# Kernel tuning notes

Measured on AMD Instinct MI355X. Metric: run time of the kernel, lower is better.

## Reference

```python
import jax, jax.numpy as jnp
import numpy as np

B, C, H, W = 4, 256, 48, 48
NUM_HEADS = 8
HEAD_DIM = C // NUM_HEADS
LN_EPS = 1e-5


def setup_inputs() -> dict:
    key = jax.random.key(0)
    ks = jax.random.split(key, 12)
    s = 1.0 / np.sqrt(C)
    return {
        "x": jax.random.normal(ks[0], (B, C, H, W), dtype=jnp.float32),
        "context": jax.random.normal(ks[1], (B, C, H, W), dtype=jnp.float32),
        "Wq": jax.random.uniform(ks[2], (C, C), jnp.float32, -s, s),
        "bq": jax.random.uniform(ks[3], (C,), jnp.float32, -s, s),
        "Wk": jax.random.uniform(ks[4], (C, C), jnp.float32, -s, s),
        "bk": jax.random.uniform(ks[5], (C,), jnp.float32, -s, s),
        "Wv": jax.random.uniform(ks[6], (C, C), jnp.float32, -s, s),
        "bv": jax.random.uniform(ks[7], (C,), jnp.float32, -s, s),
        "Wo": jax.random.uniform(ks[8], (C, C), jnp.float32, -s, s),
        "bo": jax.random.uniform(ks[9], (C,), jnp.float32, -s, s),
        "ln_w": jnp.ones((C,), jnp.float32),
        "ln_b": jnp.zeros((C,), jnp.float32),
    }


def reference(x, context, Wq, bq, Wk, bk, Wv, bv, Wo, bo, ln_w, ln_b):
    b, c, h, w = x.shape
    S = h * w
    # [B, S, C] token layout (x.view(B,C,-1).permute(0,2,1))
    x_flat = x.reshape(b, c, S).transpose(0, 2, 1)
    ctx_flat = context.reshape(b, c, S).transpose(0, 2, 1)
    # QKV projections (torch Linear: y = x @ W.T + b)
    q = (x_flat @ Wq.T + bq).reshape(b, S, NUM_HEADS, HEAD_DIM).transpose(0, 2, 1, 3)
    k = (ctx_flat @ Wk.T + bk).reshape(b, S, NUM_HEADS, HEAD_DIM).transpose(0, 2, 1, 3)
    v = (ctx_flat @ Wv.T + bv).reshape(b, S, NUM_HEADS, HEAD_DIM).transpose(0, 2, 1, 3)
    # attention: [B, heads, S, S]
    scores = jnp.einsum("bhqd,bhkd->bhqk", q, k) / np.sqrt(HEAD_DIM)
    attn = jax.nn.softmax(scores, axis=-1)  # dropout is identity in eval mode
    attended = jnp.einsum("bhqk,bhkd->bhqd", attn, v)
    attended = attended.transpose(0, 2, 1, 3).reshape(b, S, c)
    out = attended @ Wo.T + bo
    # residual + layernorm over channel dim
    y = out + x_flat
    mu = jnp.mean(y, axis=-1, keepdims=True)
    var = jnp.var(y, axis=-1, keepdims=True)
    y = (y - mu) * jax.lax.rsqrt(var + LN_EPS) * ln_w + ln_b
    return y.transpose(0, 2, 1).reshape(b, c, h, w)
```

## Files before the change

kernel.cpp:

```cpp
#include <hip/hip_runtime.h>

#define B_ 4
#define C_ 256
#define S_ 2304
#define NH_ 8
#define HD_ 32
#define QS_L2E (0.17677669529663687f * 1.4426950408889634f)

typedef __attribute__((ext_vector_type(8))) __bf16 b16x8;
typedef __attribute__((ext_vector_type(4))) __bf16 b16x4;
typedef __attribute__((ext_vector_type(4))) float f32x4;

static __device__ __forceinline__ f32x4 mfma_bf16(b16x8 a, b16x8 b, f32x4 c) {
  return __builtin_amdgcn_mfma_f32_16x16x32_bf16(a, b, c, 0, 0, 0);
}

__global__ __launch_bounds__(256) void k_cvt(
    const float* __restrict__ x, const float* __restrict__ ctx,
    const float* __restrict__ Wq, const float* __restrict__ Wk,
    const float* __restrict__ Wv, const float* __restrict__ Wo,
    __bf16* __restrict__ xT, __bf16* __restrict__ cT,
    __bf16* __restrict__ Wb, __bf16* __restrict__ Wob) {
  const int bid = blockIdx.x, t = threadIdx.x;
  if (bid < 4608) {
    __shared__ float tile[32][33];
    const int s = bid / 2304;
    int r = bid % 2304;
    const int b = r / 576; r %= 576;
    const int ct = r / 72, st = r % 72;
    const float* src = (s == 0 ? x : ctx) + ((size_t)b * C_ + ct * 32) * S_ + st * 32;
    const int tr = t >> 3, tc = (t & 7) * 4;
    f32x4 v = *(const f32x4*)(src + (size_t)tr * S_ + tc);
    tile[tr][tc] = v[0]; tile[tr][tc + 1] = v[1];
    tile[tr][tc + 2] = v[2]; tile[tr][tc + 3] = v[3];
    __syncthreads();
    __bf16* dst = (s == 0 ? xT : cT) + ((size_t)b * S_ + st * 32 + tr) * C_ + ct * 32 + tc;
    b16x4 o;
#pragma unroll
    for (int j = 0; j < 4; ++j) o[j] = (__bf16)tile[tc + j][tr];
    *(b16x4*)dst = o;
  } else {
    const int wi = bid - 4608;
    const int m = wi >> 6, chunk = wi & 63;
    const float* Wsrc = m == 0 ? Wq : (m == 1 ? Wk : (m == 2 ? Wv : Wo));
    __bf16* Wdst = (m < 3) ? (Wb + m * 65536) : Wob;
    const int e0 = chunk * 1024 + t * 4;
    f32x4 v = *(const f32x4*)(Wsrc + e0);
    b16x4 o;
#pragma unroll
    for (int j = 0; j < 4; ++j) o[j] = (__bf16)v[j];
    *(b16x4*)(Wdst + e0) = o;
  }
}

__global__ __launch_bounds__(256) void k_qkv(
    const __bf16* __restrict__ xT, const __bf16* __restrict__ cT,
    const __bf16* __restrict__ Wb,
    const float* __restrict__ bq, const float* __restrict__ bk, const float* __restrict__ bv,
    __bf16* __restrict__ Q, __bf16* __restrict__ Kd, __bf16* __restrict__ Vt) {
  const int iblk = threadIdx.x >> 6;
  const int lane = threadIdx.x & 63;
  const int col = lane & 15, g = lane >> 4;
  int r = blockIdx.x;
  const int p = r / 576; r %= 576;
  const int b = r / 144;
  const int s0 = (r % 144) * 16;
  const __bf16* src = (p == 0 ? xT : cT) + (size_t)b * S_ * C_;
  const __bf16* W = Wb + p * 65536;
  const float* bias = p == 0 ? bq : (p == 1 ? bk : bv);
  const int i0 = iblk * 64;

  f32x4 acc[4] = {};
  const __bf16* brow = src + (size_t)(s0 + col) * C_ + g * 8;
  const __bf16* arow = W + (size_t)(i0 + col) * C_ + g * 8;
#pragma unroll 2
  for (int kk = 0; kk < 8; ++kk) {
    b16x8 bf = *(const b16x8*)(brow + kk * 32);
#pragma unroll
    for (int j = 0; j < 4; ++j) {
      b16x8 af = *(const b16x8*)(arow + (size_t)j * 16 * C_ + kk * 32);
      acc[j] = mfma_bf16(af, bf, acc[j]);
    }
  }
#pragma unroll
  for (int j = 0; j < 4; ++j) {
#pragma unroll
    for (int rr = 0; rr < 4; ++rr) {
      const int i = i0 + j * 16 + g * 4 + rr;
      float val = acc[j][rr] + bias[i];
      const int h = i >> 5, d = i & 31;
      const size_t bh = (size_t)b * NH_ + h;
      if (p == 0)      Q[(bh * S_ + s0 + col) * HD_ + d] = (__bf16)(val * QS_L2E);
      else if (p == 1) Kd[(bh * S_ + s0 + col) * HD_ + d] = (__bf16)val;
      else             Vt[(bh * HD_ + d) * S_ + s0 + col] = (__bf16)val;
    }
  }
}

__global__ __launch_bounds__(192) void k_attn(
    const __bf16* __restrict__ Q, const __bf16* __restrict__ Kd,
    const __bf16* __restrict__ Vt, __bf16* __restrict__ att) {
  __shared__ float mrg[2][2][528];
  int bid = blockIdx.x;
  bid = (bid & 7) * 288 + (bid >> 3);
  const int wid = threadIdx.x >> 6;
  const int lane = threadIdx.x & 63;
  const int col = lane & 15, g = lane >> 4;
  const int bh = bid / 72;
  const int s0 = (bid % 72) * 32;
  const int b = bh >> 3, h = bh & 7;
  const __bf16* Qb = Q + (size_t)bh * S_ * HD_;
  const __bf16* Kb = Kd + (size_t)bh * S_ * HD_;
  const __bf16* Vb = Vt + (size_t)bh * HD_ * S_;

  const b16x8 qf0 = *(const b16x8*)(Qb + (s0 + col) * HD_ + g * 8);
  const b16x8 qf1 = *(const b16x8*)(Qb + (s0 + 16 + col) * HD_ + g * 8);
  const int kA = ((col >> 2) * 8) + (col & 3);
  const int kbeg = wid * (S_ / 3);

  b16x8 onesf;
#pragma unroll
  for (int j = 0; j < 8; ++j) onesf[j] = (__bf16)1.0f;

  f32x4 a00 = {}, a01 = {}, al0 = {}, a10 = {}, a11 = {}, al1 = {};
  const f32x4 zero = {};

  const __bf16* kptr = Kb + (size_t)(kbeg + kA) * HD_ + g * 8;
  const __bf16* vptr = Vb + (size_t)col * S_ + kbeg + g * 8;

  b16x8 ka = *(const b16x8*)(kptr);
  b16x8 kb = *(const b16x8*)(kptr + 4 * HD_);
  b16x8 v0 = *(const b16x8*)(vptr);
  b16x8 v1 = *(const b16x8*)(vptr + 16 * S_);

  for (int it = 0; it < S_ / 3 / 32; ++it) {
    kptr += 32 * HD_; vptr += 32;
    b16x8 ka_n = *(const b16x8*)(kptr);
    b16x8 kb_n = *(const b16x8*)(kptr + 4 * HD_);
    b16x8 v0_n = *(const b16x8*)(vptr);
    b16x8 v1_n = *(const b16x8*)(vptr + 16 * S_);
    __builtin_amdgcn_sched_barrier(0);

    f32x4 sA0 = mfma_bf16(ka, qf0, zero);
    f32x4 sB0 = mfma_bf16(kb, qf0, zero);
    f32x4 sA1 = mfma_bf16(ka, qf1, zero);
    f32x4 sB1 = mfma_bf16(kb, qf1, zero);
    b16x8 pf0, pf1;
#pragma unroll
    for (int j = 0; j < 4; ++j) {
      pf0[j]     = (__bf16)__builtin_amdgcn_exp2f(sA0[j]);
      pf0[4 + j] = (__bf16)__builtin_amdgcn_exp2f(sB0[j]);
      pf1[j]     = (__bf16)__builtin_amdgcn_exp2f(sA1[j]);
      pf1[4 + j] = (__bf16)__builtin_amdgcn_exp2f(sB1[j]);
    }
    a00 = mfma_bf16(pf0, v0, a00);
    a01 = mfma_bf16(pf0, v1, a01);
    al0 = mfma_bf16(pf0, onesf, al0);
    a10 = mfma_bf16(pf1, v0, a10);
    a11 = mfma_bf16(pf1, v1, a11);
    al1 = mfma_bf16(pf1, onesf, al1);

    ka = ka_n; kb = kb_n; v0 = v0_n; v1 = v1_n;
  }

  if (wid > 0) {
    float* m0 = mrg[wid - 1][0];
    *(f32x4*)(m0 + col * 16 + g * 4) = a00;
    *(f32x4*)(m0 + (col + 16) * 16 + g * 4) = a01;
    if (col == 0) *(f32x4*)(m0 + 512 + g * 4) = al0;
    float* m1 = mrg[wid - 1][1];
    *(f32x4*)(m1 + col * 16 + g * 4) = a10;
    *(f32x4*)(m1 + (col + 16) * 16 + g * 4) = a11;
    if (col == 0) *(f32x4*)(m1 + 512 + g * 4) = al1;
  }
  __syncthreads();
  if (wid == 0) {
#pragma unroll
    for (int qt = 0; qt < 2; ++qt) {
      const float* p0 = mrg[0][qt];
      const float* p1 = mrg[1][qt];
      f32x4 x0 = qt ? a10 : a00, x1 = qt ? a11 : a01, xl = qt ? al1 : al0;
      f32x4 o0a = *(const f32x4*)(p0 + col * 16 + g * 4);
      f32x4 o1a = *(const f32x4*)(p0 + (col + 16) * 16 + g * 4);
      f32x4 ola = *(const f32x4*)(p0 + 512 + g * 4);
      f32x4 o0b = *(const f32x4*)(p1 + col * 16 + g * 4);
      f32x4 o1b = *(const f32x4*)(p1 + (col + 16) * 16 + g * 4);
      f32x4 olb = *(const f32x4*)(p1 + 512 + g * 4);
#pragma unroll
      for (int j = 0; j < 4; ++j) {
        const int q = g * 4 + j;
        const float inv = 1.f / (xl[j] + ola[j] + olb[j]);
        const size_t obase = ((size_t)b * S_ + s0 + qt * 16 + q) * C_ + h * HD_;
        att[obase + col] = (__bf16)((x0[j] + o0a[j] + o0b[j]) * inv);
        att[obase + 16 + col] = (__bf16)((x1[j] + o1a[j] + o1b[j]) * inv);
      }
    }
  }
}

__global__ __launch_bounds__(256) void k_oln(
    const __bf16* __restrict__ att, const __bf16* __restrict__ Wob,
    const float* __restrict__ bo, const float* __restrict__ x,
    const float* __restrict__ lnw, const float* __restrict__ lnb,
    float* __restrict__ out) {
  __shared__ float part[4][2][16];
  __shared__ float lw[256], lb[256];
  const int wid = threadIdx.x >> 6;
  const int lane = threadIdx.x & 63;
  const int col = lane & 15, g = lane >> 4;
  int r = blockIdx.x;
  const int b = r / 144;
  const int s0 = (r % 144) * 16;
  const int i0 = wid * 64;
  lw[threadIdx.x] = lnw[threadIdx.x];
  lb[threadIdx.x] = lnb[threadIdx.x];

  f32x4 acc[4] = {};
  const __bf16* arow = att + ((size_t)b * S_ + s0 + col) * C_ + g * 8;
  const __bf16* wrow = Wob + (size_t)(i0 + col) * C_ + g * 8;
#pragma unroll 2
  for (int kk = 0; kk < 8; ++kk) {
    b16x8 bfr = *(const b16x8*)(arow + kk * 32);
#pragma unroll
    for (int j = 0; j < 4; ++j) {
      b16x8 af = *(const b16x8*)(wrow + (size_t)j * 16 * C_ + kk * 32);
      acc[j] = mfma_bf16(af, bfr, acc[j]);
    }
  }
  float s = 0.f, s2 = 0.f;
#pragma unroll
  for (int j = 0; j < 4; ++j) {
#pragma unroll
    for (int rr = 0; rr < 4; ++rr) {
      const int i = i0 + j * 16 + g * 4 + rr;
      float v = acc[j][rr] + bo[i] + x[((size_t)b * C_ + i) * S_ + s0 + col];
      acc[j][rr] = v;
      s += v; s2 += v * v;
    }
  }
  s += __shfl_xor(s, 16); s2 += __shfl_xor(s2, 16);
  s += __shfl_xor(s, 32); s2 += __shfl_xor(s2, 32);
  if (g == 0) { part[wid][0][col] = s; part[wid][1][col] = s2; }
  __syncthreads();
  float st = part[0][0][col] + part[1][0][col] + part[2][0][col] + part[3][0][col];
  float st2 = part[0][1][col] + part[1][1][col] + part[2][1][col] + part[3][1][col];
  const float mu = st * (1.f / 256.f);
  const float rs = rsqrtf(st2 * (1.f / 256.f) - mu * mu + 1e-5f);
#pragma unroll
  for (int j = 0; j < 4; ++j) {
#pragma unroll
    for (int rr = 0; rr < 4; ++rr) {
      const int i = i0 + j * 16 + g * 4 + rr;
      out[((size_t)b * C_ + i) * S_ + s0 + col] = (acc[j][rr] - mu) * rs * lw[i] + lb[i];
    }
  }
}

extern "C" void kernel_launch(void* const* d_in, const int* in_sizes, int n_in,
                              void* d_out, int out_size, void* d_ws, size_t ws_size,
                              hipStream_t stream) {
  const float* x   = (const float*)d_in[0];
  const float* ctx = (const float*)d_in[1];
  const float* Wq  = (const float*)d_in[2];
  const float* bq  = (const float*)d_in[3];
  const float* Wk  = (const float*)d_in[4];
  const float* bk  = (const float*)d_in[5];
  const float* Wv  = (const float*)d_in[6];
  const float* bv  = (const float*)d_in[7];
  const float* Wo  = (const float*)d_in[8];
  const float* bo  = (const float*)d_in[9];
  const float* lnw = (const float*)d_in[10];
  const float* lnb = (const float*)d_in[11];
  float* out = (float*)d_out;

  char* ws = (char*)d_ws;
  __bf16* xT  = (__bf16*)(ws);
  __bf16* cT  = (__bf16*)(ws + 4718592);
  __bf16* Wb  = (__bf16*)(ws + 9437184);
  __bf16* Wob = (__bf16*)(ws + 9830400);
  __bf16* Q   = (__bf16*)(ws + 9961472);
  __bf16* Kd  = (__bf16*)(ws + 14680064);
  __bf16* Vt  = (__bf16*)(ws + 19398656);
  __bf16* att = (__bf16*)(ws + 24117248);

  k_cvt  <<<4864, 256, 0, stream>>>(x, ctx, Wq, Wk, Wv, Wo, xT, cT, Wb, Wob);
  k_qkv  <<<1728, 256, 0, stream>>>(xT, cT, Wb, bq, bk, bv, Q, Kd, Vt);
  k_attn <<<2304, 192, 0, stream>>>(Q, Kd, Vt, att);
  k_oln  <<< 576, 256, 0, stream>>>(att, Wob, bo, x, lnw, lnb, out);
}
```

Before: 215.0 us.

## Enlarge per-block tiles across kernels and software-pipeline GEMM loads

The attention kernel now processes 64 queries per block instead of 32, so each K/V fragment load feeds four query tiles. The QKV GEMM computes 32 tokens per block with register double-buffered operand prefetch, and the output GEMM also gains explicit prefetch. The conversion kernel does four tiles per block to cut block count. Workspace buffers are reordered. The aim is to raise data reuse and hide load latency, at the cost of more registers and fewer blocks, which could lower occupancy.

```diff
diff --git a/kernel.cpp b/kernel.cpp
--- a/kernel.cpp
+++ b/kernel.cpp
@@ -22,34 +22,43 @@
     __bf16* __restrict__ xT, __bf16* __restrict__ cT,
     __bf16* __restrict__ Wb, __bf16* __restrict__ Wob) {
   const int bid = blockIdx.x, t = threadIdx.x;
-  if (bid < 4608) {
+  if (bid < 1152) {
     __shared__ float tile[32][33];
-    const int s = bid / 2304;
-    int r = bid % 2304;
-    const int b = r / 576; r %= 576;
-    const int ct = r / 72, st = r % 72;
-    const float* src = (s == 0 ? x : ctx) + ((size_t)b * C_ + ct * 32) * S_ + st * 32;
     const int tr = t >> 3, tc = (t & 7) * 4;
-    f32x4 v = *(const f32x4*)(src + (size_t)tr * S_ + tc);
-    tile[tr][tc] = v[0]; tile[tr][tc + 1] = v[1];
-    tile[tr][tc + 2] = v[2]; tile[tr][tc + 3] = v[3];
-    __syncthreads();
-    __bf16* dst = (s == 0 ? xT : cT) + ((size_t)b * S_ + st * 32 + tr) * C_ + ct * 32 + tc;
-    b16x4 o;
-#pragma unroll
-    for (int j = 0; j < 4; ++j) o[j] = (__bf16)tile[tc + j][tr];
-    *(b16x4*)dst = o;
+#pragma unroll
+    for (int i = 0; i < 4; ++i) {
+      const int tid4 = bid * 4 + i;
+      const int s = tid4 / 2304;
+      int r = tid4 % 2304;
+      const int b = r / 576; r %= 576;
+      const int ct = r / 72, st = r % 72;
+      const float* src = (s == 0 ? x : ctx) + ((size_t)b * C_ + ct * 32) * S_ + st * 32;
+      if (i) __syncthreads();
+      f32x4 v = *(const f32x4*)(src + (size_t)tr * S_ + tc);
+      tile[tr][tc] = v[0]; tile[tr][tc + 1] = v[1];
+      tile[tr][tc + 2] = v[2]; tile[tr][tc + 3] = v[3];
+      __syncthreads();
+      __bf16* dst = (s == 0 ? xT : cT) + ((size_t)b * S_ + st * 32 + tr) * C_ + ct * 32 + tc;
+      b16x4 o;
+#pragma unroll
+      for (int j = 0; j < 4; ++j) o[j] = (__bf16)tile[tc + j][tr];
+      *(b16x4*)dst = o;
+    }
   } else {
-    const int wi = bid - 4608;
-    const int m = wi >> 6, chunk = wi & 63;
-    const float* Wsrc = m == 0 ? Wq : (m == 1 ? Wk : (m == 2 ? Wv : Wo));
-    __bf16* Wdst = (m < 3) ? (Wb + m * 65536) : Wob;
-    const int e0 = chunk * 1024 + t * 4;
-    f32x4 v = *(const f32x4*)(Wsrc + e0);
-    b16x4 o;
-#pragma unroll
-    for (int j = 0; j < 4; ++j) o[j] = (__bf16)v[j];
-    *(b16x4*)(Wdst + e0) = o;
+    const int bid2 = bid - 1152;
+#pragma unroll
+    for (int i = 0; i < 4; ++i) {
+      const int wi = bid2 * 4 + i;
+      const int m = wi >> 6, chunk = wi & 63;
+      const float* Wsrc = m == 0 ? Wq : (m == 1 ? Wk : (m == 2 ? Wv : Wo));
+      __bf16* Wdst = (m < 3) ? (Wb + m * 65536) : Wob;
+      const int e0 = chunk * 1024 + t * 4;
+      f32x4 v = *(const f32x4*)(Wsrc + e0);
+      b16x4 o;
+#pragma unroll
+      for (int j = 0; j < 4; ++j) o[j] = (__bf16)v[j];
+      *(b16x4*)(Wdst + e0) = o;
+    }
   }
 }
 
@@ -62,37 +71,60 @@
   const int lane = threadIdx.x & 63;
   const int col = lane & 15, g = lane >> 4;
   int r = blockIdx.x;
-  const int p = r / 576; r %= 576;
-  const int b = r / 144;
-  const int s0 = (r % 144) * 16;
+  const int p = r / 288; r %= 288;
+  const int b = r / 72;
+  const int s0 = (r % 72) * 32;
   const __bf16* src = (p == 0 ? xT : cT) + (size_t)b * S_ * C_;
   const __bf16* W = Wb + p * 65536;
   const float* bias = p == 0 ? bq : (p == 1 ? bk : bv);
   const int i0 = iblk * 64;
 
-  f32x4 acc[4] = {};
-  const __bf16* brow = src + (size_t)(s0 + col) * C_ + g * 8;
+  f32x4 acc[2][4] = {};
+  const __bf16* brow0 = src + (size_t)(s0 + col) * C_ + g * 8;
+  const __bf16* brow1 = brow0 + 16 * C_;
   const __bf16* arow = W + (size_t)(i0 + col) * C_ + g * 8;
-#pragma unroll 2
+
+  b16x8 bf0 = *(const b16x8*)(brow0);
+  b16x8 bf1 = *(const b16x8*)(brow1);
+  b16x8 af0 = *(const b16x8*)(arow);
+  b16x8 af1 = *(const b16x8*)(arow + (size_t)16 * C_);
+  b16x8 af2 = *(const b16x8*)(arow + (size_t)32 * C_);
+  b16x8 af3 = *(const b16x8*)(arow + (size_t)48 * C_);
+
   for (int kk = 0; kk < 8; ++kk) {
-    b16x8 bf = *(const b16x8*)(brow + kk * 32);
+    const int nk = (kk + 1) * 32;
+    b16x8 nbf0 = *(const b16x8*)(brow0 + nk);
+    b16x8 nbf1 = *(const b16x8*)(brow1 + nk);
+    b16x8 naf0 = *(const b16x8*)(arow + nk);
+    b16x8 naf1 = *(const b16x8*)(arow + (size_t)16 * C_ + nk);
+    b16x8 naf2 = *(const b16x8*)(arow + (size_t)32 * C_ + nk);
+    b16x8 naf3 = *(const b16x8*)(arow + (size_t)48 * C_ + nk);
+    __builtin_amdgcn_sched_barrier(0);
+    acc[0][0] = mfma_bf16(af0, bf0, acc[0][0]);
+    acc[0][1] = mfma_bf16(af1, bf0, acc[0][1]);
+    acc[0][2] = mfma_bf16(af2, bf0, acc[0][2]);
+    acc[0][3] = mfma_bf16(af3, bf0, acc[0][3]);
+    acc[1][0] = mfma_bf16(af0, bf1, acc[1][0]);
+    acc[1][1] = mfma_bf16(af1, bf1, acc[1][1]);
+    acc[1][2] = mfma_bf16(af2, bf1, acc[1][2]);
+    acc[1][3] = mfma_bf16(af3, bf1, acc[1][3]);
+    bf0 = nbf0; bf1 = nbf1; af0 = naf0; af1 = naf1; af2 = naf2; af3 = naf3;
+  }
+#pragma unroll
+  for (int tf = 0; tf < 2; ++tf) {
 #pragma unroll
     for (int j = 0; j < 4; ++j) {
-      b16x8 af = *(const b16x8*)(arow + (size_t)j * 16 * C_ + kk * 32);
-      acc[j] = mfma_bf16(af, bf, acc[j]);
-    }
-  }
-#pragma unroll
-  for (int j = 0; j < 4; ++j) {
-#pragma unroll
-    for (int rr = 0; rr < 4; ++rr) {
-      const int i = i0 + j * 16 + g * 4 + rr;
-      float val = acc[j][rr] + bias[i];
-      const int h = i >> 5, d = i & 31;
-      const size_t bh = (size_t)b * NH_ + h;
-      if (p == 0)      Q[(bh * S_ + s0 + col) * HD_ + d] = (__bf16)(val * QS_L2E);
-      else if (p == 1) Kd[(bh * S_ + s0 + col) * HD_ + d] = (__bf16)val;
-      else             Vt[(bh * HD_ + d) * S_ + s0 + col] = (__bf16)val;
+#pragma unroll
+      for (int rr = 0; rr < 4; ++rr) {
+        const int i = i0 + j * 16 + g * 4 + rr;
+        float val = acc[tf][j][rr] + bias[i];
+        const int h = i >> 5, d = i & 31;
+        const size_t bh = (size_t)b * NH_ + h;
+        const int tok = s0 + tf * 16 + col;
+        if (p == 0)      Q[(bh * S_ + tok) * HD_ + d] = (__bf16)(val * QS_L2E);
+        else if (p == 1) Kd[(bh * S_ + tok) * HD_ + d] = (__bf16)val;
+        else             Vt[(bh * HD_ + d) * S_ + tok] = (__bf16)val;
+      }
     }
   }
 }
@@ -100,21 +132,23 @@
 __global__ __launch_bounds__(192) void k_attn(
     const __bf16* __restrict__ Q, const __bf16* __restrict__ Kd,
     const __bf16* __restrict__ Vt, __bf16* __restrict__ att) {
-  __shared__ float mrg[2][2][528];
+  __shared__ float mrg[2][4][528];
   int bid = blockIdx.x;
-  bid = (bid & 7) * 288 + (bid >> 3);
+  bid = (bid & 7) * 144 + (bid >> 3);
   const int wid = threadIdx.x >> 6;
   const int lane = threadIdx.x & 63;
   const int col = lane & 15, g = lane >> 4;
-  const int bh = bid / 72;
-  const int s0 = (bid % 72) * 32;
+  const int bh = bid / 36;
+  const int s0 = (bid % 36) * 64;
   const int b = bh >> 3, h = bh & 7;
   const __bf16* Qb = Q + (size_t)bh * S_ * HD_;
   const __bf16* Kb = Kd + (size_t)bh * S_ * HD_;
   const __bf16* Vb = Vt + (size_t)bh * HD_ * S_;
 
-  const b16x8 qf0 = *(const b16x8*)(Qb + (s0 + col) * HD_ + g * 8);
-  const b16x8 qf1 = *(const b16x8*)(Qb + (s0 + 16 + col) * HD_ + g * 8);
+  b16x8 qfr[4];
+#pragma unroll
+  for (int q = 0; q < 4; ++q)
+    qfr[q] = *(const b16x8*)(Qb + (size_t)(s0 + q * 16 + col) * HD_ + g * 8);
   const int kA = ((col >> 2) * 8) + (col & 3);
   const int kbeg = wid * (S_ / 3);
 
@@ -122,7 +156,7 @@
 #pragma unroll
   for (int j = 0; j < 8; ++j) onesf[j] = (__bf16)1.0f;
 
-  f32x4 a00 = {}, a01 = {}, al0 = {}, a10 = {}, a11 = {}, al1 = {};
+  f32x4 acc0[4] = {}, acc1[4] = {}, accl[4] = {};
   const f32x4 zero = {};
 
   const __bf16* kptr = Kb + (size_t)(kbeg + kA) * HD_ + g * 8;
@@ -141,45 +175,38 @@
     b16x8 v1_n = *(const b16x8*)(vptr + 16 * S_);
     __builtin_amdgcn_sched_barrier(0);
 
-    f32x4 sA0 = mfma_bf16(ka, qf0, zero);
-    f32x4 sB0 = mfma_bf16(kb, qf0, zero);
-    f32x4 sA1 = mfma_bf16(ka, qf1, zero);
-    f32x4 sB1 = mfma_bf16(kb, qf1, zero);
-    b16x8 pf0, pf1;
-#pragma unroll
-    for (int j = 0; j < 4; ++j) {
-      pf0[j]     = (__bf16)__builtin_amdgcn_exp2f(sA0[j]);
-      pf0[4 + j] = (__bf16)__builtin_amdgcn_exp2f(sB0[j]);
-      pf1[j]     = (__bf16)__builtin_amdgcn_exp2f(sA1[j]);
-      pf1[4 + j] = (__bf16)__builtin_amdgcn_exp2f(sB1[j]);
-    }
-    a00 = mfma_bf16(pf0, v0, a00);
-    a01 = mfma_bf16(pf0, v1, a01);
-    al0 = mfma_bf16(pf0, onesf, al0);
-    a10 = mfma_bf16(pf1, v0, a10);
-    a11 = mfma_bf16(pf1, v1, a11);
-    al1 = mfma_bf16(pf1, onesf, al1);
-
+#pragma unroll
+    for (int q = 0; q < 4; ++q) {
+      f32x4 sA = mfma_bf16(ka, qfr[q], zero);
+      f32x4 sB = mfma_bf16(kb, qfr[q], zero);
+      b16x8 pf;
+#pragma unroll
+      for (int j = 0; j < 4; ++j) {
+        pf[j]     = (__bf16)__builtin_amdgcn_exp2f(sA[j]);
+        pf[4 + j] = (__bf16)__builtin_amdgcn_exp2f(sB[j]);
+      }
+      acc0[q] = mfma_bf16(pf, v0, acc0[q]);
+      acc1[q] = mfma_bf16(pf, v1, acc1[q]);
+      accl[q] = mfma_bf16(pf, onesf, accl[q]);
+    }
     ka = ka_n; kb = kb_n; v0 = v0_n; v1 = v1_n;
   }
 
   if (wid > 0) {
-    float* m0 = mrg[wid - 1][0];
-    *(f32x4*)(m0 + col * 16 + g * 4) = a00;
-    *(f32x4*)(m0 + (col + 16) * 16 + g * 4) = a01;
-    if (col == 0) *(f32x4*)(m0 + 512 + g * 4) = al0;
-    float* m1 = mrg[wid - 1][1];
-    *(f32x4*)(m1 + col * 16 + g * 4) = a10;
-    *(f32x4*)(m1 + (col + 16) * 16 + g * 4) = a11;
-    if (col == 0) *(f32x4*)(m1 + 512 + g * 4) = al1;
+#pragma unroll
+    for (int qt = 0; qt < 4; ++qt) {
+      float* m0 = mrg[wid - 1][qt];
+      *(f32x4*)(m0 + col * 16 + g * 4) = acc0[qt];
+      *(f32x4*)(m0 + (col + 16) * 16 + g * 4) = acc1[qt];
+      if (col == 0) *(f32x4*)(m0 + 512 + g * 4) = accl[qt];
+    }
   }
   __syncthreads();
   if (wid == 0) {
 #pragma unroll
-    for (int qt = 0; qt < 2; ++qt) {
+    for (int qt = 0; qt < 4; ++qt) {
       const float* p0 = mrg[0][qt];
       const float* p1 = mrg[1][qt];
-      f32x4 x0 = qt ? a10 : a00, x1 = qt ? a11 : a01, xl = qt ? al1 : al0;
       f32x4 o0a = *(const f32x4*)(p0 + col * 16 + g * 4);
       f32x4 o1a = *(const f32x4*)(p0 + (col + 16) * 16 + g * 4);
       f32x4 ola = *(const f32x4*)(p0 + 512 + g * 4);
@@ -189,10 +216,10 @@
 #pragma unroll
       for (int j = 0; j < 4; ++j) {
         const int q = g * 4 + j;
-        const float inv = 1.f / (xl[j] + ola[j] + olb[j]);
+        const float inv = 1.f / (accl[qt][j] + ola[j] + olb[j]);
         const size_t obase = ((size_t)b * S_ + s0 + qt * 16 + q) * C_ + h * HD_;
-        att[obase + col] = (__bf16)((x0[j] + o0a[j] + o0b[j]) * inv);
-        att[obase + 16 + col] = (__bf16)((x1[j] + o1a[j] + o1b[j]) * inv);
+        att[obase + col] = (__bf16)((acc0[qt][j] + o0a[j] + o0b[j]) * inv);
+        att[obase + 16 + col] = (__bf16)((acc1[qt][j] + o1a[j] + o1b[j]) * inv);
       }
     }
   }
@@ -218,14 +245,26 @@
   f32x4 acc[4] = {};
   const __bf16* arow = att + ((size_t)b * S_ + s0 + col) * C_ + g * 8;
   const __bf16* wrow = Wob + (size_t)(i0 + col) * C_ + g * 8;
-#pragma unroll 2
+
+  b16x8 bfr = *(const b16x8*)(arow);
+  b16x8 af0 = *(const b16x8*)(wrow);
+  b16x8 af1 = *(const b16x8*)(wrow + (size_t)16 * C_);
+  b16x8 af2 = *(const b16x8*)(wrow + (size_t)32 * C_);
+  b16x8 af3 = *(const b16x8*)(wrow + (size_t)48 * C_);
+
   for (int kk = 0; kk < 8; ++kk) {
-    b16x8 bfr = *(const b16x8*)(arow + kk * 32);
-#pragma unroll
-    for (int j = 0; j < 4; ++j) {
-      b16x8 af = *(const b16x8*)(wrow + (size_t)j * 16 * C_ + kk * 32);
-      acc[j] = mfma_bf16(af, bfr, acc[j]);
-    }
+    const int nk = (kk + 1) * 32;
+    b16x8 nbfr = *(const b16x8*)(arow + nk);
+    b16x8 naf0 = *(const b16x8*)(wrow + nk);
+    b16x8 naf1 = *(const b16x8*)(wrow + (size_t)16 * C_ + nk);
+    b16x8 naf2 = *(const b16x8*)(wrow + (size_t)32 * C_ + nk);
+    b16x8 naf3 = *(const b16x8*)(wrow + (size_t)48 * C_ + nk);
+    __builtin_amdgcn_sched_barrier(0);
+    acc[0] = mfma_bf16(af0, bfr, acc[0]);
+    acc[1] = mfma_bf16(af1, bfr, acc[1]);
+    acc[2] = mfma_bf16(af2, bfr, acc[2]);
+    acc[3] = mfma_bf16(af3, bfr, acc[3]);
+    bfr = nbfr; af0 = naf0; af1 = naf1; af2 = naf2; af3 = naf3;
   }
   float s = 0.f, s2 = 0.f;
 #pragma unroll
@@ -278,13 +317,13 @@
   __bf16* cT  = (__bf16*)(ws + 4718592);
   __bf16* Wb  = (__bf16*)(ws + 9437184);
   __bf16* Wob = (__bf16*)(ws + 9830400);
-  __bf16* Q   = (__bf16*)(ws + 9961472);
-  __bf16* Kd  = (__bf16*)(ws + 14680064);
-  __bf16* Vt  = (__bf16*)(ws + 19398656);
-  __bf16* att = (__bf16*)(ws + 24117248);
-
-  k_cvt  <<<4864, 256, 0, stream>>>(x, ctx, Wq, Wk, Wv, Wo, xT, cT, Wb, Wob);
-  k_qkv  <<<1728, 256, 0, stream>>>(xT, cT, Wb, bq, bk, bv, Q, Kd, Vt);
-  k_attn <<<2304, 192, 0, stream>>>(Q, Kd, Vt, att);
+  __bf16* Kd  = (__bf16*)(ws + 9961472);
+  __bf16* Vt  = (__bf16*)(ws + 14680064);
+  __bf16* att = (__bf16*)(ws + 19398656);
+  __bf16* Q   = (__bf16*)(ws + 24117248);
+
+  k_cvt  <<<1216, 256, 0, stream>>>(x, ctx, Wq, Wk, Wv, Wo, xT, cT, Wb, Wob);
+  k_qkv  <<< 864, 256, 0, stream>>>(xT, cT, Wb, bq, bk, bv, Q, Kd, Vt);
+  k_attn <<<1152, 192, 0, stream>>>(Q, Kd, Vt, att);
   k_oln  <<< 576, 256, 0, stream>>>(att, Wob, bo, x, lnw, lnb, out);
 }
```

After: 191.9 us. -10.7%, faster.
